# Kernel optimization log

Measured on AMD Instinct MI355X. Metric: run time of the kernel, lower is better.

The kernel has to match this reference:

```python
import jax, jax.numpy as jnp
import numpy as np
import math

B, S, U, H = 8, 1024, 1024, 16
DK = U // H  # 64


def setup_inputs() -> dict:
    key = jax.random.key(0)
    ks = jax.random.split(key, 12)
    query = jax.random.normal(ks[0], (B, S, U), jnp.float32)
    key_t = jax.random.normal(ks[1], (B, S, U), jnp.float32)  # unused by module (bug preserved)
    value = jax.random.normal(ks[2], (B, S, U), jnp.float32)  # unused by module (bug preserved)
    # causal multiplicative 0/1 mask [B,S,S]
    mask = jnp.broadcast_to(jnp.tril(jnp.ones((S, S), jnp.float32)), (B, S, S))
    bh = math.sqrt(1.0 / DK)   # init bound for per-head projections (out_features=d_k)
    bo = math.sqrt(1.0 / U)    # init bound for output projection (out_features=n_units)
    u = lambda k, shape, b: jax.random.uniform(k, shape, jnp.float32, -b, b)
    # per-head weights stacked: [H, U, DK] (already input->output layout)
    Wq = u(ks[3], (H, U, DK), bh); bq = u(ks[4], (H, DK), bh)
    Wk = u(ks[5], (H, U, DK), bh); bk = u(ks[6], (H, DK), bh)
    Wv = u(ks[7], (H, U, DK), bh); bv = u(ks[8], (H, DK), bh)
    Wo = u(ks[9], (U, U), bo);     bo_ = u(ks[10], (U,), bo)
    return dict(query=query, key=key_t, value=value, mask=mask,
                Wq=Wq, bq=bq, Wk=Wk, bk=bk, Wv=Wv, bv=bv, Wo=Wo, bo=bo_)


def reference(query, key, value, mask, Wq, bq, Wk, bk, Wv, bv, Wo, bo):
    # NOTE: faithful to source — q, k, v are ALL projected from `query`.
    q = jnp.einsum('bsu,hud->bhsd', query, Wq) + bq[:, None, :]
    k = jnp.einsum('bsu,hud->bhsd', query, Wk) + bk[:, None, :]
    v = jnp.einsum('bsu,hud->bhsd', query, Wv) + bv[:, None, :]
    scores = jnp.einsum('bhqd,bhkd->bhqk', q, k) / math.sqrt(DK)
    s = mask[:, None, :, :]  # broadcast over heads
    x = scores * s - 1e9 * (1.0 - s)  # multiplicative mask baked into softmax input
    attn = jax.nn.softmax(x, axis=-1)
    out = jnp.einsum('bhqk,bhkd->bhqd', attn, v)
    # concat heads along feature dim (head 0 first, matching torch.cat order)
    out = out.transpose(0, 2, 1, 3).reshape(B, S, U)
    return out @ Wo + bo
```

## Files before the change

kernel.cpp:

```cpp
#include <hip/hip_runtime.h>
#include <hip/hip_bf16.h>

#define B_ 8
#define S_ 1024
#define U_ 1024
#define H_ 16
#define DK_ 64

typedef __attribute__((ext_vector_type(8))) short short8;
typedef __attribute__((ext_vector_type(4))) float f32x4;
typedef __attribute__((ext_vector_type(16))) float f32x16;

__device__ inline ushort f2b(float x) {
  union { float f; unsigned u; } v; v.f = x;
  unsigned r = (v.u + 0x7FFFu + ((v.u >> 16) & 1u)) >> 16;
  return (ushort)r;
}
__device__ inline unsigned pk2(float lo, float hi) {
  return (unsigned)f2b(lo) | ((unsigned)f2b(hi) << 16);
}

__device__ inline void gld16(const ushort* g, ushort* l) {
  __builtin_amdgcn_global_load_lds((__attribute__((address_space(1))) void*)(g),
                                   (__attribute__((address_space(3))) void*)(l),
                                   16, 0, 0);
}

__global__ __launch_bounds__(256) void pack_x_kern(const float* __restrict__ X,
                                                   ushort* __restrict__ Xb) {
  int idx = blockIdx.x * 256 + threadIdx.x;
  const float4* src = (const float4*)X + (size_t)idx * 2;
  float4 a = src[0], b = src[1];
  ushort r[8];
  r[0]=f2b(a.x); r[1]=f2b(a.y); r[2]=f2b(a.z); r[3]=f2b(a.w);
  r[4]=f2b(b.x); r[5]=f2b(b.y); r[6]=f2b(b.z); r[7]=f2b(b.w);
  *(uint4*)(Xb + (size_t)idx*8) = *(uint4*)r;
}

__global__ __launch_bounds__(256) void pack_w_kern(
    const float* __restrict__ Wq, const float* __restrict__ Wk, const float* __restrict__ Wv,
    const float* __restrict__ bq, const float* __restrict__ bk, const float* __restrict__ bv,
    const float* __restrict__ Wo,
    ushort* __restrict__ Wqkv, float* __restrict__ Bqkv, ushort* __restrict__ Wob)
{
  __shared__ ushort tile[64*65];
  const int t = threadIdx.x;
  const int bid = blockIdx.x;
  if (bid < 768) {
    int p = bid >> 8, rem = bid & 255;
    int h = rem >> 4, kc = rem & 15, k0 = kc*64;
    const float* Wsrc = (p==0) ? Wq : ((p==1) ? Wk : Wv);
    #pragma unroll
    for (int i = 0; i < 16; ++i) {
      int e = t + i*256;
      int r = e >> 6, d = e & 63;
      tile[d*65 + r] = f2b(Wsrc[h*65536 + (k0+r)*64 + d]);
    }
    __syncthreads();
    #pragma unroll
    for (int i = 0; i < 16; ++i) {
      int e = t + i*256;
      int d = e >> 6, r = e & 63;
      Wqkv[(size_t)(p*1024 + h*64 + d)*1024 + k0 + r] = tile[d*65 + r];
    }
    if (kc == 0 && t < 64) {
      const float* bsrc = (p==0) ? bq : ((p==1) ? bk : bv);
      Bqkv[p*1024 + h*64 + t] = bsrc[h*64 + t];
    }
  } else {
    int b2 = bid - 768;
    int nc = b2 >> 4, kc = b2 & 15;
    int n0 = nc*64, k0 = kc*64;
    #pragma unroll
    for (int i = 0; i < 16; ++i) {
      int e = t + i*256;
      int r = e >> 6, d = e & 63;
      tile[d*65 + r] = f2b(Wo[(size_t)(k0+r)*1024 + n0 + d]);
    }
    __syncthreads();
    #pragma unroll
    for (int i = 0; i < 16; ++i) {
      int e = t + i*256;
      int d = e >> 6, r = e & 63;
      Wob[(size_t)(n0+d)*1024 + k0 + r] = tile[d*65 + r];
    }
  }
}

template<int MODE>
__global__ __launch_bounds__(256, 2) void gemm128_kern(
    const ushort* __restrict__ A,
    const ushort* __restrict__ Bw,
    const float* __restrict__ bias,
    ushort* __restrict__ Qb, ushort* __restrict__ Kb, ushort* __restrict__ Vtb,
    float* __restrict__ outF)
{
  __shared__ __align__(16) ushort As[2][8192];
  __shared__ __align__(16) ushort Bs[2][8192];

  const int t = threadIdx.x;
  const int l = t & 63, w = t >> 6;
  const int wr = w >> 1, wc = w & 1;
  const int li = l & 15, c4 = l >> 4;

  int m0, n0;
  if (MODE==0) {
    int swz = (blockIdx.x & 7) * 192 + (blockIdx.x >> 3);
    int ms = swz / 192, rem = swz % 192;
    m0 = (ms*8 + (rem & 7)) * 128;  n0 = (rem >> 3) * 128;
  } else {
    int swz = (blockIdx.x & 7) * 64 + (blockIdx.x >> 3);
    int ms = swz / 64, rem = swz % 64;
    m0 = (ms*8 + (rem & 7)) * 128;  n0 = (rem >> 3) * 128;
  }

  f32x4 acc[4][4];
  #pragma unroll
  for (int i=0;i<4;i++)
    #pragma unroll
    for (int j=0;j<4;j++) acc[i][j] = (f32x4)0.0f;

  auto SA = [&](int buf, int kk) {
    #pragma unroll
    for (int p=0;p<4;++p) {
      int n = p*256 + t;
      int row = n >> 3, jj = (n & 7) ^ (row & 7);
      gld16(&A[(size_t)(m0 + row)*1024 + kk + jj*8], &As[buf][n*8]);
    }
  };
  auto SB = [&](int buf, int kk) {
    #pragma unroll
    for (int p=0;p<4;++p) {
      int n = p*256 + t;
      int row = n >> 3, jj = (n & 7) ^ (row & 7);
      gld16(&Bw[(size_t)(n0 + row)*1024 + kk + jj*8], &Bs[buf][n*8]);
    }
  };

  SA(0, 0);  SB(0, 0);
  SA(1, 64); SB(1, 64);
  asm volatile("s_waitcnt vmcnt(8)" ::: "memory");
  __builtin_amdgcn_s_barrier();
  __builtin_amdgcn_sched_barrier(0);

  for (int kt = 0; kt < 16; ++kt) {
    const int cur = kt & 1;
    short8 af[4][2], bf[4][2];
    #pragma unroll
    for (int i=0;i<4;i++) {
      int rA = wr*64 + i*16 + li;
      int rB = wc*64 + i*16 + li;
      #pragma unroll
      for (int ks=0;ks<2;ks++) {
        af[i][ks] = *(const short8*)&As[cur][rA*64 + (((ks*4+c4)^(li&7))*8)];
        bf[i][ks] = *(const short8*)&Bs[cur][rB*64 + (((ks*4+c4)^(li&7))*8)];
      }
    }
    __builtin_amdgcn_s_setprio(1);
    #pragma unroll
    for (int i=0;i<4;i++)
      #pragma unroll
      for (int j=0;j<4;j++)
        #pragma unroll
        for (int ks=0;ks<2;ks++)
          acc[i][j] = __builtin_amdgcn_mfma_f32_16x16x32_bf16(af[i][ks], bf[j][ks], acc[i][j], 0,0,0);
    __builtin_amdgcn_s_setprio(0);

    __builtin_amdgcn_s_barrier();
    __builtin_amdgcn_sched_barrier(0);
    const int kk2 = ((kt + 2) & 15) * 64;
    SA(cur, kk2); SB(cur, kk2);
    asm volatile("s_waitcnt vmcnt(8)" ::: "memory");
    __builtin_amdgcn_s_barrier();
    __builtin_amdgcn_sched_barrier(0);
  }

  #pragma unroll
  for (int i=0;i<4;i++) {
    int rbase = m0 + wr*64 + i*16 + c4*4;
    #pragma unroll
    for (int j=0;j<4;j++) {
      int col = n0 + wc*64 + j*16 + li;
      float bv = bias[col];
      if (MODE == 0) {
        int p = col >> 10, h = (col >> 6) & 15, d = col & 63;
        int b = rbase >> 10, s = rbase & 1023;
        if (p == 2) {
          ushort pk4[4];
          #pragma unroll
          for (int r=0;r<4;r++) pk4[r] = f2b(acc[i][j][r] + bv);
          *(uint2*)&Vtb[((size_t)((b*16+h)*64 + d))*1024 + s] = *(uint2*)pk4;
        } else {
          ushort* dst = (p==0) ? Qb : Kb;
          float sc = (p==0) ? 0.18033688011112042f : 1.0f;
          #pragma unroll
          for (int r=0;r<4;r++)
            dst[(((size_t)(b*16 + h))*1024 + s + r)*64 + d] = f2b((acc[i][j][r] + bv) * sc);
        }
      } else {
        #pragma unroll
        for (int r=0;r<4;r++)
          outF[(size_t)(rbase+r)*1024 + col] = acc[i][j][r] + bv;
      }
    }
  }
}

__global__ __launch_bounds__(256, 3) void attn_kern(
    const ushort* __restrict__ Qb, const ushort* __restrict__ Kb,
    const ushort* __restrict__ Vt, ushort* __restrict__ Ob)
{
  __shared__ __align__(16) ushort Pb[4][32*40];
  __shared__ __align__(16) ushort OT[4][32*72];
  const int t = threadIdx.x, l = t & 63, w = t >> 6;
  const int bid = blockIdx.x;
  const int x = bid & 7, i0 = bid >> 3;
  const int bh = x*16 + (i0 >> 3), j = i0 & 7;
  int qt;
  if      (w == 0) qt = j;
  else if (w == 1) qt = 15 - j;
  else if (w == 2) qt = 16 + j;
  else             qt = 31 - j;

  const int col = l & 31, hi = l >> 5;
  const ushort* Qp = Qb + (size_t)bh*65536;
  const ushort* Kp = Kb + (size_t)bh*65536;
  const ushort* Vp = Vt + (size_t)bh*65536;

  short8 qf[4];
  #pragma unroll
  for (int m=0;m<4;m++)
    qf[m] = *(const short8*)&Qp[(size_t)(qt*32+col)*64 + m*16 + hi*8];

  f32x16 accO0 = (f32x16)0.0f, accO1 = (f32x16)0.0f;
  float mR = -1e30f, lS = 0.0f;

  ushort* Pw = &Pb[w][0];
  const int nt = qt + 1;
  for (int kt = 0; kt < nt; ++kt) {
    short8 kf[4], vf0[2], vf1[2];
    #pragma unroll
    for (int m=0;m<4;m++)
      kf[m] = *(const short8*)&Kp[(size_t)(kt*32+col)*64 + m*16 + hi*8];
    #pragma unroll
    for (int m=0;m<2;m++) {
      vf0[m] = *(const short8*)&Vp[(size_t)col*1024      + kt*32 + m*16 + hi*8];
      vf1[m] = *(const short8*)&Vp[(size_t)(32+col)*1024 + kt*32 + m*16 + hi*8];
    }

    f32x16 s = (f32x16)0.0f;
    #pragma unroll
    for (int m=0;m<4;m++)
      s = __builtin_amdgcn_mfma_f32_32x32x16_bf16(kf[m], qf[m], s, 0, 0, 0);

    if (kt == qt) {
      #pragma unroll
      for (int r=0;r<16;r++) {
        int kvl = (r&3) + ((r>>2)<<3) + 4*hi;
        s[r] = (kvl > col) ? -1e9f : s[r];
      }
    }

    float mx = s[0];
    #pragma unroll
    for (int r=1;r<16;r++) mx = fmaxf(mx, s[r]);
    mx = fmaxf(mx, __shfl_xor(mx, 32));

    if (__any(mx - mR > 8.0f)) {
      float mN = fmaxf(mR, mx);
      float corr = __builtin_amdgcn_exp2f(mR - mN);
      mR = mN; lS *= corr;
      #pragma unroll
      for (int r=0;r<16;r++) { accO0[r] *= corr; accO1[r] *= corr; }
    }

    float p[16], rs = 0.0f;
    #pragma unroll
    for (int r=0;r<16;r++) { p[r] = __builtin_amdgcn_exp2f(s[r] - mR); rs += p[r]; }
    rs += __shfl_xor(rs, 32);
    lS += rs;

    #pragma unroll
    for (int r2=0;r2<8;r2++) {
      int r = 2*r2;
      int kv = (r&3) + ((r>>2)<<3) + 4*hi;
      *(unsigned*)&Pw[col*40 + kv] = pk2(p[r], p[r+1]);
    }
    short8 pb0 = *(const short8*)&Pw[col*40 + hi*8];
    short8 pb1 = *(const short8*)&Pw[col*40 + 16 + hi*8];

    accO0 = __builtin_amdgcn_mfma_f32_32x32x16_bf16(vf0[0], pb0, accO0, 0,0,0);
    accO0 = __builtin_amdgcn_mfma_f32_32x32x16_bf16(vf0[1], pb1, accO0, 0,0,0);
    accO1 = __builtin_amdgcn_mfma_f32_32x32x16_bf16(vf1[0], pb0, accO1, 0,0,0);
    accO1 = __builtin_amdgcn_mfma_f32_32x32x16_bf16(vf1[1], pb1, accO1, 0,0,0);
  }

  float inv = 1.0f / lS;
  ushort* o = &OT[w][0];
  #pragma unroll
  for (int r2=0;r2<8;r2++) {
    int r = 2*r2;
    int dv = (r&3) + ((r>>2)<<3) + 4*hi;
    *(unsigned*)&o[col*72 + dv]      = pk2(accO0[r]*inv, accO0[r+1]*inv);
    *(unsigned*)&o[col*72 + 32 + dv] = pk2(accO1[r]*inv, accO1[r+1]*inv);
  }
  const int b = bh >> 4, h = bh & 15;
  #pragma unroll
  for (int it=0; it<4; ++it) {
    int q = it*8 + (l>>3), c8 = (l&7)*8;
    uint4 v = *(const uint4*)&o[q*72 + c8];
    int qg = qt*32 + q;
    *(uint4*)&Ob[(size_t)(b*1024+qg)*1024 + h*64 + c8] = v;
  }
}

extern "C" void kernel_launch(void* const* d_in, const int* in_sizes, int n_in,
                              void* d_out, int out_size, void* d_ws, size_t ws_size,
                              hipStream_t stream) {
  const float* query = (const float*)d_in[0];
  const float* Wq = (const float*)d_in[4];
  const float* bq = (const float*)d_in[5];
  const float* Wk = (const float*)d_in[6];
  const float* bk = (const float*)d_in[7];
  const float* Wv = (const float*)d_in[8];
  const float* bv = (const float*)d_in[9];
  const float* Wo = (const float*)d_in[10];
  const float* bo = (const float*)d_in[11];

  char* wsb = (char*)d_ws;
  ushort* Xb   = (ushort*)(wsb);
  ushort* Wqkv = (ushort*)(wsb + 16777216);
  float*  Bqkv = (float*) (wsb + 23068672);
  ushort* Wob  = (ushort*)(wsb + 23080960);
  ushort* Qb   = (ushort*)(wsb + 25178112);
  ushort* Kb   = (ushort*)(wsb + 41955328);
  ushort* Vtb  = (ushort*)(wsb + 58732544);
  ushort* Ob   = (ushort*)(wsb + 75509760);

  hipLaunchKernelGGL(pack_x_kern, dim3(4096), dim3(256), 0, stream, query, Xb);
  hipLaunchKernelGGL(pack_w_kern, dim3(1024), dim3(256), 0, stream,
                     Wq, Wk, Wv, bq, bk, bv, Wo, Wqkv, Bqkv, Wob);
  hipLaunchKernelGGL(gemm128_kern<0>, dim3(1536), dim3(256), 0, stream,
                     Xb, Wqkv, Bqkv, Qb, Kb, Vtb, (float*)nullptr);
  hipLaunchKernelGGL(attn_kern, dim3(1024), dim3(256), 0, stream, Qb, Kb, Vtb, Ob);
  hipLaunchKernelGGL(gemm128_kern<1>, dim3(512), dim3(256), 0, stream,
                     Ob, Wob, bo, (ushort*)nullptr, (ushort*)nullptr, (ushort*)nullptr,
                     (float*)d_out);
}
```

Before: 168.3 us.

## Pair causal query tiles per wave in attention and halve GEMM K-tile

The attention kernel now gives each wave two query tiles (p and 31-p), so the causal workload is balanced and each K/V tile fetched from global memory feeds both tiles. The grid shrinks to 512 blocks and the occupancy hint drops to 2. Separately, the GEMM uses 32-wide K tiles with a 4-slot swizzle, halving LDS use so the occupancy hint can rise to 4, and moves the wait and barrier to the top of each iteration. The costs are more registers per attention wave and twice as many GEMM iterations, each with its own barriers.

Result: no change. 167.8 us (-0.3%).

```diff
diff --git a/kernel.cpp b/kernel.cpp
--- a/kernel.cpp
+++ b/kernel.cpp
@@ -88,15 +88,15 @@
 }
 
 template<int MODE>
-__global__ __launch_bounds__(256, 2) void gemm128_kern(
+__global__ __launch_bounds__(256, 4) void gemm128_kern(
     const ushort* __restrict__ A,
     const ushort* __restrict__ Bw,
     const float* __restrict__ bias,
     ushort* __restrict__ Qb, ushort* __restrict__ Kb, ushort* __restrict__ Vtb,
     float* __restrict__ outF)
 {
-  __shared__ __align__(16) ushort As[2][8192];
-  __shared__ __align__(16) ushort Bs[2][8192];
+  __shared__ __align__(16) ushort As[2][4096];
+  __shared__ __align__(16) ushort Bs[2][4096];
 
   const int t = threadIdx.x;
   const int l = t & 63, w = t >> 6;
@@ -122,57 +122,50 @@
 
   auto SA = [&](int buf, int kk) {
     #pragma unroll
-    for (int p=0;p<4;++p) {
-      int n = p*256 + t;
-      int row = n >> 3, jj = (n & 7) ^ (row & 7);
+    for (int p2=0;p2<2;++p2) {
+      int n = p2*256 + t;
+      int row = n >> 2, jj = (n & 3) ^ ((row >> 1) & 3);
       gld16(&A[(size_t)(m0 + row)*1024 + kk + jj*8], &As[buf][n*8]);
     }
   };
   auto SB = [&](int buf, int kk) {
     #pragma unroll
-    for (int p=0;p<4;++p) {
-      int n = p*256 + t;
-      int row = n >> 3, jj = (n & 7) ^ (row & 7);
+    for (int p2=0;p2<2;++p2) {
+      int n = p2*256 + t;
+      int row = n >> 2, jj = (n & 3) ^ ((row >> 1) & 3);
       gld16(&Bw[(size_t)(n0 + row)*1024 + kk + jj*8], &Bs[buf][n*8]);
     }
   };
 
   SA(0, 0);  SB(0, 0);
-  SA(1, 64); SB(1, 64);
-  asm volatile("s_waitcnt vmcnt(8)" ::: "memory");
-  __builtin_amdgcn_s_barrier();
-  __builtin_amdgcn_sched_barrier(0);
-
-  for (int kt = 0; kt < 16; ++kt) {
+  SA(1, 32); SB(1, 32);
+
+  for (int kt = 0; kt < 32; ++kt) {
     const int cur = kt & 1;
-    short8 af[4][2], bf[4][2];
+    asm volatile("s_waitcnt vmcnt(4)" ::: "memory");
+    __builtin_amdgcn_s_barrier();
+    __builtin_amdgcn_sched_barrier(0);
+
+    short8 af[4], bf[4];
     #pragma unroll
     for (int i=0;i<4;i++) {
       int rA = wr*64 + i*16 + li;
       int rB = wc*64 + i*16 + li;
-      #pragma unroll
-      for (int ks=0;ks<2;ks++) {
-        af[i][ks] = *(const short8*)&As[cur][rA*64 + (((ks*4+c4)^(li&7))*8)];
-        bf[i][ks] = *(const short8*)&Bs[cur][rB*64 + (((ks*4+c4)^(li&7))*8)];
-      }
+      af[i] = *(const short8*)&As[cur][rA*32 + ((c4 ^ ((rA>>1)&3))*8)];
+      bf[i] = *(const short8*)&Bs[cur][rB*32 + ((c4 ^ ((rB>>1)&3))*8)];
     }
     __builtin_amdgcn_s_setprio(1);
     #pragma unroll
     for (int i=0;i<4;i++)
       #pragma unroll
       for (int j=0;j<4;j++)
-        #pragma unroll
-        for (int ks=0;ks<2;ks++)
-          acc[i][j] = __builtin_amdgcn_mfma_f32_16x16x32_bf16(af[i][ks], bf[j][ks], acc[i][j], 0,0,0);
+        acc[i][j] = __builtin_amdgcn_mfma_f32_16x16x32_bf16(af[i], bf[j], acc[i][j], 0,0,0);
     __builtin_amdgcn_s_setprio(0);
 
     __builtin_amdgcn_s_barrier();
     __builtin_amdgcn_sched_barrier(0);
-    const int kk2 = ((kt + 2) & 15) * 64;
+    const int kk2 = ((kt + 2) & 31) * 32;
     SA(cur, kk2); SB(cur, kk2);
-    asm volatile("s_waitcnt vmcnt(8)" ::: "memory");
-    __builtin_amdgcn_s_barrier();
-    __builtin_amdgcn_sched_barrier(0);
   }
 
   #pragma unroll
@@ -206,7 +199,7 @@
   }
 }
 
-__global__ __launch_bounds__(256, 3) void attn_kern(
+__global__ __launch_bounds__(256, 2) void attn_kern(
     const ushort* __restrict__ Qb, const ushort* __restrict__ Kb,
     const ushort* __restrict__ Vt, ushort* __restrict__ Ob)
 {
@@ -215,103 +208,113 @@
   const int t = threadIdx.x, l = t & 63, w = t >> 6;
   const int bid = blockIdx.x;
   const int x = bid & 7, i0 = bid >> 3;
-  const int bh = x*16 + (i0 >> 3), j = i0 & 7;
-  int qt;
-  if      (w == 0) qt = j;
-  else if (w == 1) qt = 15 - j;
-  else if (w == 2) qt = 16 + j;
-  else             qt = 31 - j;
+  const int bh = x*16 + (i0 >> 2);
+  const int p  = (i0 & 3)*4 + w;
+  const int qta = p, qtb = 31 - p;
 
   const int col = l & 31, hi = l >> 5;
   const ushort* Qp = Qb + (size_t)bh*65536;
   const ushort* Kp = Kb + (size_t)bh*65536;
   const ushort* Vp = Vt + (size_t)bh*65536;
 
-  short8 qf[4];
+  short8 qfa[4], qfb[4];
   #pragma unroll
-  for (int m=0;m<4;m++)
-    qf[m] = *(const short8*)&Qp[(size_t)(qt*32+col)*64 + m*16 + hi*8];
-
-  f32x16 accO0 = (f32x16)0.0f, accO1 = (f32x16)0.0f;
-  float mR = -1e30f, lS = 0.0f;
-
+  for (int m=0;m<4;m++) {
+    qfa[m] = *(const short8*)&Qp[(size_t)(qta*32+col)*64 + m*16 + hi*8];
+    qfb[m] = *(const short8*)&Qp[(size_t)(qtb*32+col)*64 + m*16 + hi*8];
+  }
+
+  f32x16 aA0 = (f32x16)0.0f, aA1 = (f32x16)0.0f;
+  f32x16 aB0 = (f32x16)0.0f, aB1 = (f32x16)0.0f;
+  float mA = -1e30f, lA = 0.0f, mB = -1e30f, lB = 0.0f;
   ushort* Pw = &Pb[w][0];
-  const int nt = qt + 1;
-  for (int kt = 0; kt < nt; ++kt) {
-    short8 kf[4], vf0[2], vf1[2];
-    #pragma unroll
-    for (int m=0;m<4;m++)
-      kf[m] = *(const short8*)&Kp[(size_t)(kt*32+col)*64 + m*16 + hi*8];
-    #pragma unroll
-    for (int m=0;m<2;m++) {
-      vf0[m] = *(const short8*)&Vp[(size_t)col*1024      + kt*32 + m*16 + hi*8];
-      vf1[m] = *(const short8*)&Vp[(size_t)(32+col)*1024 + kt*32 + m*16 + hi*8];
-    }
-
-    f32x16 s = (f32x16)0.0f;
-    #pragma unroll
-    for (int m=0;m<4;m++)
-      s = __builtin_amdgcn_mfma_f32_32x32x16_bf16(kf[m], qf[m], s, 0, 0, 0);
-
-    if (kt == qt) {
+
+  auto PROC = [&](f32x16& s, bool diag, float& mR, float& lS,
+                  f32x16& o0, f32x16& o1, const short8* vf0, const short8* vf1) {
+    if (diag) {
       #pragma unroll
       for (int r=0;r<16;r++) {
         int kvl = (r&3) + ((r>>2)<<3) + 4*hi;
         s[r] = (kvl > col) ? -1e9f : s[r];
       }
     }
-
     float mx = s[0];
     #pragma unroll
     for (int r=1;r<16;r++) mx = fmaxf(mx, s[r]);
     mx = fmaxf(mx, __shfl_xor(mx, 32));
-
     if (__any(mx - mR > 8.0f)) {
       float mN = fmaxf(mR, mx);
       float corr = __builtin_amdgcn_exp2f(mR - mN);
       mR = mN; lS *= corr;
       #pragma unroll
-      for (int r=0;r<16;r++) { accO0[r] *= corr; accO1[r] *= corr; }
-    }
-
-    float p[16], rs = 0.0f;
-    #pragma unroll
-    for (int r=0;r<16;r++) { p[r] = __builtin_amdgcn_exp2f(s[r] - mR); rs += p[r]; }
+      for (int r=0;r<16;r++) { o0[r] *= corr; o1[r] *= corr; }
+    }
+    float pr[16], rs = 0.0f;
+    #pragma unroll
+    for (int r=0;r<16;r++) { pr[r] = __builtin_amdgcn_exp2f(s[r] - mR); rs += pr[r]; }
     rs += __shfl_xor(rs, 32);
     lS += rs;
-
     #pragma unroll
     for (int r2=0;r2<8;r2++) {
       int r = 2*r2;
       int kv = (r&3) + ((r>>2)<<3) + 4*hi;
-      *(unsigned*)&Pw[col*40 + kv] = pk2(p[r], p[r+1]);
+      *(unsigned*)&Pw[col*40 + kv] = pk2(pr[r], pr[r+1]);
     }
     short8 pb0 = *(const short8*)&Pw[col*40 + hi*8];
     short8 pb1 = *(const short8*)&Pw[col*40 + 16 + hi*8];
-
-    accO0 = __builtin_amdgcn_mfma_f32_32x32x16_bf16(vf0[0], pb0, accO0, 0,0,0);
-    accO0 = __builtin_amdgcn_mfma_f32_32x32x16_bf16(vf0[1], pb1, accO0, 0,0,0);
-    accO1 = __builtin_amdgcn_mfma_f32_32x32x16_bf16(vf1[0], pb0, accO1, 0,0,0);
-    accO1 = __builtin_amdgcn_mfma_f32_32x32x16_bf16(vf1[1], pb1, accO1, 0,0,0);
-  }
-
-  float inv = 1.0f / lS;
-  ushort* o = &OT[w][0];
-  #pragma unroll
-  for (int r2=0;r2<8;r2++) {
-    int r = 2*r2;
-    int dv = (r&3) + ((r>>2)<<3) + 4*hi;
-    *(unsigned*)&o[col*72 + dv]      = pk2(accO0[r]*inv, accO0[r+1]*inv);
-    *(unsigned*)&o[col*72 + 32 + dv] = pk2(accO1[r]*inv, accO1[r+1]*inv);
-  }
+    o0 = __builtin_amdgcn_mfma_f32_32x32x16_bf16(vf0[0], pb0, o0, 0,0,0);
+    o0 = __builtin_amdgcn_mfma_f32_32x32x16_bf16(vf0[1], pb1, o0, 0,0,0);
+    o1 = __builtin_amdgcn_mfma_f32_32x32x16_bf16(vf1[0], pb0, o1, 0,0,0);
+    o1 = __builtin_amdgcn_mfma_f32_32x32x16_bf16(vf1[1], pb1, o1, 0,0,0);
+  };
+
+  for (int kt = 0; kt <= qtb; ++kt) {
+    short8 kf[4], vf0[2], vf1[2];
+    #pragma unroll
+    for (int m=0;m<4;m++)
+      kf[m] = *(const short8*)&Kp[(size_t)(kt*32+col)*64 + m*16 + hi*8];
+    #pragma unroll
+    for (int m=0;m<2;m++) {
+      vf0[m] = *(const short8*)&Vp[(size_t)col*1024      + kt*32 + m*16 + hi*8];
+      vf1[m] = *(const short8*)&Vp[(size_t)(32+col)*1024 + kt*32 + m*16 + hi*8];
+    }
+
+    f32x16 sB = (f32x16)0.0f;
+    #pragma unroll
+    for (int m=0;m<4;m++)
+      sB = __builtin_amdgcn_mfma_f32_32x32x16_bf16(kf[m], qfb[m], sB, 0, 0, 0);
+    PROC(sB, kt == qtb, mB, lB, aB0, aB1, vf0, vf1);
+
+    if (kt <= qta) {
+      f32x16 sA = (f32x16)0.0f;
+      #pragma unroll
+      for (int m=0;m<4;m++)
+        sA = __builtin_amdgcn_mfma_f32_32x32x16_bf16(kf[m], qfa[m], sA, 0, 0, 0);
+      PROC(sA, kt == qta, mA, lA, aA0, aA1, vf0, vf1);
+    }
+  }
+
   const int b = bh >> 4, h = bh & 15;
-  #pragma unroll
-  for (int it=0; it<4; ++it) {
-    int q = it*8 + (l>>3), c8 = (l&7)*8;
-    uint4 v = *(const uint4*)&o[q*72 + c8];
-    int qg = qt*32 + q;
-    *(uint4*)&Ob[(size_t)(b*1024+qg)*1024 + h*64 + c8] = v;
-  }
+  auto EPI = [&](int qt, float lS, const f32x16& o0, const f32x16& o1) {
+    float inv = 1.0f / lS;
+    ushort* o = &OT[w][0];
+    #pragma unroll
+    for (int r2=0;r2<8;r2++) {
+      int r = 2*r2;
+      int dv = (r&3) + ((r>>2)<<3) + 4*hi;
+      *(unsigned*)&o[col*72 + dv]      = pk2(o0[r]*inv, o0[r+1]*inv);
+      *(unsigned*)&o[col*72 + 32 + dv] = pk2(o1[r]*inv, o1[r+1]*inv);
+    }
+    #pragma unroll
+    for (int it=0; it<4; ++it) {
+      int q = it*8 + (l>>3), c8 = (l&7)*8;
+      uint4 v = *(const uint4*)&o[q*72 + c8];
+      int qg = qt*32 + q;
+      *(uint4*)&Ob[(size_t)(b*1024+qg)*1024 + h*64 + c8] = v;
+    }
+  };
+  EPI(qta, lA, aA0, aA1);
+  EPI(qtb, lB, aB0, aB1);
 }
 
 extern "C" void kernel_launch(void* const* d_in, const int* in_sizes, int n_in,
@@ -342,7 +345,7 @@
                      Wq, Wk, Wv, bq, bk, bv, Wo, Wqkv, Bqkv, Wob);
   hipLaunchKernelGGL(gemm128_kern<0>, dim3(1536), dim3(256), 0, stream,
                      Xb, Wqkv, Bqkv, Qb, Kb, Vtb, (float*)nullptr);
-  hipLaunchKernelGGL(attn_kern, dim3(1024), dim3(256), 0, stream, Qb, Kb, Vtb, Ob);
+  hipLaunchKernelGGL(attn_kern, dim3(512), dim3(256), 0, stream, Qb, Kb, Vtb, Ob);
   hipLaunchKernelGGL(gemm128_kern<1>, dim3(512), dim3(256), 0, stream,
                      Ob, Wob, bo, (ushort*)nullptr, (ushort*)nullptr, (ushort*)nullptr,
                      (float*)d_out);
```
